# Performance work log

Hardware: AMD Instinct MI355X
Metric: run time of the kernel (lower is better)

The kernel has to match this reference:

```python
import jax, jax.numpy as jnp
import numpy as np

DT = 0.001
TAU_SYN = 0.01
TAU_MEM = 0.005
THRESHOLD = 1.0
ALPHA = float(np.exp(-DT / TAU_SYN))  # syn decay
BETA = float(np.exp(-DT / TAU_MEM))   # mem decay

BATCH, IN_SIZE, OUT_SIZE = 4096, 2048, 2048


@jax.custom_vjp
def spike(x):
    # Heaviside forward with sigmoid-derivative surrogate gradient
    return (x > 0).astype(x.dtype)

def _spike_fwd(x):
    return spike(x), x

def _spike_bwd(x, g):
    s = jax.nn.sigmoid(x)
    return (g * s * (1.0 - s),)

spike.defvjp(_spike_fwd, _spike_bwd)


def setup_inputs() -> dict:
    key = jax.random.key(0)
    k1, k2, k3, k4, k5 = jax.random.split(key, 5)
    inputs = jax.random.normal(k1, (BATCH, IN_SIZE), dtype=jnp.float32)
    I = jax.random.normal(k2, (BATCH, OUT_SIZE), dtype=jnp.float32)
    V = jax.random.normal(k3, (BATCH, OUT_SIZE), dtype=jnp.float32)
    Z = jnp.zeros((BATCH, OUT_SIZE), dtype=jnp.float32)
    # initialize_weights_: ndim<=2 -> normal init
    fwd_w = jax.random.normal(k4, (IN_SIZE, OUT_SIZE), dtype=jnp.float32)
    rec_w = jax.random.normal(k5, (OUT_SIZE, OUT_SIZE), dtype=jnp.float32)
    return {"inputs": inputs, "I": I, "V": V, "Z": Z,
            "fwd_w": fwd_w, "rec_w": rec_w}


def reference(inputs, I, V, Z, fwd_w, rec_w):
    # LIFLayer.forward_Erme, single timestep
    input_current = jnp.matmul(inputs, fwd_w)          # [B, O]
    rec_current = jnp.matmul(Z, rec_w)                 # [B, O]
    is_active = 1.0 - jax.lax.stop_gradient(Z)
    next_I = ALPHA * I + input_current + rec_current
    next_V = (BETA * V + next_I) * is_active
    next_Z = spike(next_V - THRESHOLD)
    return next_Z, next_I, next_V
```

## Files before the change

kernel.cpp:

```cpp
#include <hip/hip_runtime.h>
#include <cstdint>
#include <cstddef>

typedef __bf16 bf16_t;
typedef __bf16 bf16x4 __attribute__((ext_vector_type(4)));
typedef __bf16 bf16x8 __attribute__((ext_vector_type(8)));
typedef float f32x4 __attribute__((ext_vector_type(4)));

#define M_DIM 4096
#define K_DIM 2048
#define N_DIM 2048

#define BM 128
#define BN 128
#define BK 64
#define KT (K_DIM / BK)
#define A_EL (BM * BK)
#define B_EL (BN * BK)
#define PER_BUF (A_EL + B_EL)
#define B_OFF A_EL

#define ZCAP 64

#define MFMA16(a, b, c) \
  __builtin_amdgcn_mfma_f32_16x16x32_bf16((a), (b), (c), 0, 0, 0)

__device__ __forceinline__ void gload_lds16(const bf16_t* g, bf16_t* l) {
  __builtin_amdgcn_global_load_lds(
      (const __attribute__((address_space(1))) void*)g,
      (__attribute__((address_space(3))) void*)l, 16, 0, 0);
}

__global__ __launch_bounds__(256) void prepass_all(
    const float* __restrict__ inputs, const float* __restrict__ fwd_w,
    const float* __restrict__ Z, bf16_t* __restrict__ abf,
    bf16_t* __restrict__ wT, int* __restrict__ zcnt, int* __restrict__ zidx,
    float* __restrict__ zval) {
  __shared__ float tile[64][65];
  const int b = blockIdx.x;
  const int t = threadIdx.x;

  if (b < 4096) {
    const size_t base = ((size_t)b * 256 + t) * 8;
    const float4 v0 = *reinterpret_cast<const float4*>(inputs + base);
    const float4 v1 = *reinterpret_cast<const float4*>(inputs + base + 4);
    bf16x8 o;
    o[0] = (bf16_t)v0.x; o[1] = (bf16_t)v0.y;
    o[2] = (bf16_t)v0.z; o[3] = (bf16_t)v0.w;
    o[4] = (bf16_t)v1.x; o[5] = (bf16_t)v1.y;
    o[6] = (bf16_t)v1.z; o[7] = (bf16_t)v1.w;
    *reinterpret_cast<bf16x8*>(abf + base) = o;
  } else if (b < 5120) {
    const int bb = b - 4096;
    const int n0 = (bb & 31) * 64;
    const int k0 = (bb >> 5) * 64;
#pragma unroll
    for (int p = 0; p < 4; ++p) {
      const int r = p * 16 + (t >> 4);
      const int c = (t & 15) * 4;
      const float4 v = *reinterpret_cast<const float4*>(
          &fwd_w[(size_t)(k0 + r) * N_DIM + n0 + c]);
      tile[r][c + 0] = v.x;
      tile[r][c + 1] = v.y;
      tile[r][c + 2] = v.z;
      tile[r][c + 3] = v.w;
    }
    __syncthreads();
#pragma unroll
    for (int p = 0; p < 4; ++p) {
      const int n = p * 16 + (t >> 4);
      const int c = (t & 15) * 4;
      bf16x4 o;
      o[0] = (bf16_t)tile[c + 0][n];
      o[1] = (bf16_t)tile[c + 1][n];
      o[2] = (bf16_t)tile[c + 2][n];
      o[3] = (bf16_t)tile[c + 3][n];
      *reinterpret_cast<bf16x4*>(&wT[(size_t)(n0 + n) * K_DIM + k0 + c]) = o;
    }
  } else {
    const int row = (b - 5120) * 4 + (t >> 6);
    const int lane = t & 63;
    const float* zr = Z + (size_t)row * N_DIM;
    int local = 0;
#pragma unroll
    for (int c = 0; c < 32; c += 4) {
      const f32x4 v = *reinterpret_cast<const f32x4*>(zr + lane * 32 + c);
#pragma unroll
      for (int e = 0; e < 4; ++e) local += (v[e] != 0.0f) ? 1 : 0;
    }
    int pre = local;
#pragma unroll
    for (int d = 1; d < 64; d <<= 1) {
      const int up = __shfl_up(pre, d, 64);
      if (lane >= d) pre += up;
    }
    const int total = __shfl(pre, 63, 64);
    if (lane == 0) zcnt[row] = total;
    if (total > 0 && total <= ZCAP) {
      int wpos = pre - local;
      int* zi = zidx + (size_t)row * ZCAP;
      float* zv = zval + (size_t)row * ZCAP;
      for (int c = lane * 32; c < lane * 32 + 32; ++c) {
        const float v = zr[c];
        if (v != 0.0f) {
          zi[wpos] = c;
          zv[wpos] = v;
          ++wpos;
        }
      }
    }
  }
}

__global__ __launch_bounds__(256, 2) void lif_gemm_db(
    const bf16_t* __restrict__ A, const bf16_t* __restrict__ W,
    const float* __restrict__ recw,
    const int* __restrict__ zcnt, const int* __restrict__ zidx,
    const float* __restrict__ zval,
    const float* __restrict__ Iin, const float* __restrict__ Vin,
    const float* __restrict__ Zin,
    float* __restrict__ outZ, float* __restrict__ outI,
    float* __restrict__ outV) {
  __shared__ __align__(16) bf16_t lds[2 * PER_BUF];

  const int tid = threadIdx.x;
  const int lane = tid & 63;
  const int wave = tid >> 6;
  const int wm = wave >> 1;
  const int wn = wave & 1;
  const int l15 = lane & 15;
  const int l4 = lane >> 4;

  const int bid = blockIdx.x;
  const int swz = (bid & 7) * 64 + (bid >> 3);
  const int m0 = (swz >> 4) * BM;
  const int n0 = (swz & 15) * BN;

  const int lr = lane >> 3;
  const int sg = (lane & 7) ^ lr;
  const bf16_t* aSrc[4];
  const bf16_t* bSrc[4];
  int aDst[4], bDst[4];
#pragma unroll
  for (int i = 0; i < 4; ++i) {
    const int r = wave * 32 + i * 8 + lr;
    aSrc[i] = A + (size_t)(m0 + r) * K_DIM + sg * 8;
    aDst[i] = r * BK + (lane & 7) * 8;
    bSrc[i] = W + (size_t)(n0 + r) * K_DIM + sg * 8;
    bDst[i] = B_OFF + r * BK + (lane & 7) * 8;
  }

  int aBase[2], bBase[2];
#pragma unroll
  for (int ks = 0; ks < 2; ++ks) {
    const int phys = (l4 + ks * 4) ^ (l15 & 7);
    aBase[ks] = (wm * 64 + l15) * BK + phys * 8;
    bBase[ks] = B_OFF + (wn * 64 + l15) * BK + phys * 8;
  }

  f32x4 acc[4][4];
#pragma unroll
  for (int i = 0; i < 4; ++i)
#pragma unroll
    for (int j = 0; j < 4; ++j)
#pragma unroll
      for (int e = 0; e < 4; ++e) acc[i][j][e] = 0.0f;

#pragma unroll
  for (int i = 0; i < 4; ++i) {
    gload_lds16(aSrc[i], lds + aDst[i]);
    gload_lds16(bSrc[i], lds + bDst[i]);
  }
#pragma unroll
  for (int i = 0; i < 4; ++i) {
    gload_lds16(aSrc[i] + BK, lds + PER_BUF + aDst[i]);
    gload_lds16(bSrc[i] + BK, lds + PER_BUF + bDst[i]);
  }
  asm volatile("s_waitcnt vmcnt(8)" ::: "memory");
  __builtin_amdgcn_sched_barrier(0);
  __builtin_amdgcn_s_barrier();
  __builtin_amdgcn_sched_barrier(0);

  for (int t = 0; t < KT; ++t) {
    const bf16_t* bufC = lds + (t & 1) * PER_BUF;
    bf16_t* bufS = lds + (t & 1) * PER_BUF;

    bf16x8 af[4][2], bfr[4][2];
#pragma unroll
    for (int mi = 0; mi < 4; ++mi)
#pragma unroll
      for (int ks = 0; ks < 2; ++ks)
        af[mi][ks] =
            *reinterpret_cast<const bf16x8*>(bufC + aBase[ks] + mi * 1024);
#pragma unroll
    for (int ni = 0; ni < 4; ++ni)
#pragma unroll
      for (int ks = 0; ks < 2; ++ks)
        bfr[ni][ks] =
            *reinterpret_cast<const bf16x8*>(bufC + bBase[ks] + ni * 1024);
    asm volatile("s_waitcnt lgkmcnt(0)" ::: "memory");
    __builtin_amdgcn_sched_barrier(0);
    __builtin_amdgcn_s_barrier();
    __builtin_amdgcn_sched_barrier(0);

    if (t + 2 < KT) {
      const int kt = (t + 2) * BK;
#pragma unroll
      for (int i = 0; i < 4; ++i) {
        gload_lds16(aSrc[i] + kt, bufS + aDst[i]);
        gload_lds16(bSrc[i] + kt, bufS + bDst[i]);
      }
    }

    __builtin_amdgcn_s_setprio(1);
#pragma unroll
    for (int mi = 0; mi < 4; ++mi)
#pragma unroll
      for (int ni = 0; ni < 4; ++ni) {
        acc[mi][ni] = MFMA16(af[mi][0], bfr[ni][0], acc[mi][ni]);
        acc[mi][ni] = MFMA16(af[mi][1], bfr[ni][1], acc[mi][ni]);
      }
    __builtin_amdgcn_s_setprio(0);
    __builtin_amdgcn_sched_barrier(0);

    if (t + 2 < KT) {
      asm volatile("s_waitcnt vmcnt(8)" ::: "memory");
    } else if (t + 1 < KT) {
      asm volatile("s_waitcnt vmcnt(0)" ::: "memory");
    }
    __builtin_amdgcn_sched_barrier(0);
    __builtin_amdgcn_s_barrier();
    __builtin_amdgcn_sched_barrier(0);
  }

  const float alpha = 0.90483741803595957f;
  const float beta = 0.81873075307798182f;
  float* swp = reinterpret_cast<float*>(lds) + wave * (16 * 66);
  const int er = lane >> 2;
  const int ec = (lane & 3) * 4;

#pragma unroll
  for (int mi = 0; mi < 4; ++mi) {
#pragma unroll
    for (int ni = 0; ni < 4; ++ni)
#pragma unroll
      for (int j = 0; j < 4; ++j)
        swp[(l4 * 4 + j) * 66 + ni * 16 + l15] = acc[mi][ni][j];

    const int row = m0 + wm * 64 + mi * 16 + er;
    const int colb = n0 + wn * 64 + ec;
    const int cnt = zcnt[row];

    f32x4 rec4[4], gate4[4];
#pragma unroll
    for (int cc = 0; cc < 4; ++cc)
#pragma unroll
      for (int e = 0; e < 4; ++e) {
        rec4[cc][e] = 0.0f;
        gate4[cc][e] = 1.0f;
      }
    if (cnt > 0) {
      if (cnt <= ZCAP) {
        const int* zi = zidx + (size_t)row * ZCAP;
        const float* zv = zval + (size_t)row * ZCAP;
        for (int s = 0; s < cnt; ++s) {
          const int o = zi[s];
          const float v = zv[s];
          const float* wr = recw + (size_t)o * N_DIM + colb;
#pragma unroll
          for (int cc = 0; cc < 4; ++cc) {
            const f32x4 wv = *reinterpret_cast<const f32x4*>(wr + cc * 16);
#pragma unroll
            for (int e = 0; e < 4; ++e) {
              rec4[cc][e] += v * wv[e];
              gate4[cc][e] = (o == colb + cc * 16 + e) ? (1.0f - v)
                                                       : gate4[cc][e];
            }
          }
        }
      } else {
        const float* zr = Zin + (size_t)row * N_DIM;
        for (int o = 0; o < N_DIM; ++o) {
          const float v = zr[o];
          if (v != 0.0f) {
            const float* wr = recw + (size_t)o * N_DIM + colb;
#pragma unroll
            for (int cc = 0; cc < 4; ++cc) {
              const f32x4 wv = *reinterpret_cast<const f32x4*>(wr + cc * 16);
#pragma unroll
              for (int e = 0; e < 4; ++e) {
                rec4[cc][e] += v * wv[e];
                gate4[cc][e] = (o == colb + cc * 16 + e) ? (1.0f - v)
                                                         : gate4[cc][e];
              }
            }
          }
        }
      }
    }

    const size_t gb = (size_t)row * N_DIM + colb;
#pragma unroll
    for (int cc = 0; cc < 4; ++cc) {
      const f32x4 av =
          *reinterpret_cast<const f32x4*>(swp + er * 66 + ec + cc * 16);
      const f32x4 iv = *reinterpret_cast<const f32x4*>(Iin + gb + cc * 16);
      const f32x4 vv = *reinterpret_cast<const f32x4*>(Vin + gb + cc * 16);
      f32x4 nI, nV, nZ;
#pragma unroll
      for (int e = 0; e < 4; ++e) {
        nI[e] = alpha * iv[e] + av[e] + rec4[cc][e];
        nV[e] = (beta * vv[e] + nI[e]) * gate4[cc][e];
        nZ[e] = (nV[e] > 1.0f) ? 1.0f : 0.0f;
      }
      *reinterpret_cast<f32x4*>(outI + gb + cc * 16) = nI;
      *reinterpret_cast<f32x4*>(outV + gb + cc * 16) = nV;
      *reinterpret_cast<f32x4*>(outZ + gb + cc * 16) = nZ;
    }
  }
}

extern "C" void kernel_launch(void* const* d_in, const int* in_sizes, int n_in,
                              void* d_out, int out_size, void* d_ws,
                              size_t ws_size, hipStream_t stream) {
  const float* inputs = (const float*)d_in[0];
  const float* I = (const float*)d_in[1];
  const float* V = (const float*)d_in[2];
  const float* Z = (const float*)d_in[3];
  const float* fwd_w = (const float*)d_in[4];
  const float* rec_w = (const float*)d_in[5];

  float* outZ = (float*)d_out;
  float* outI = outZ + (size_t)M_DIM * N_DIM;
  float* outV = outI + (size_t)M_DIM * N_DIM;

  bf16_t* abf = (bf16_t*)d_ws;
  bf16_t* wT = (bf16_t*)((char*)d_ws + (size_t)M_DIM * K_DIM * 2);
  char* p = (char*)d_ws + (size_t)M_DIM * K_DIM * 2 + (size_t)N_DIM * K_DIM * 2;
  int* zcnt = (int*)p;
  int* zidx = (int*)(p + M_DIM * 4);
  float* zval = (float*)(p + M_DIM * 4 + (size_t)M_DIM * ZCAP * 4);

  hipLaunchKernelGGL(prepass_all, dim3(6144), dim3(256), 0, stream, inputs,
                     fwd_w, Z, abf, wT, zcnt, zidx, zval);
  hipLaunchKernelGGL(lif_gemm_db, dim3((M_DIM / BM) * (N_DIM / BN)),
                     dim3(256), 0, stream, abf, wT, rec_w, zcnt, zidx, zval, I,
                     V, Z, outZ, outI, outV);
}
```

Measured before the change: 85.87 us.

## Replace 4-wave 128x128 GEMM tiles with single-wave 64x64 tiles

```diff
diff --git a/kernel.cpp b/kernel.cpp
--- a/kernel.cpp
+++ b/kernel.cpp
@@ -11,13 +11,12 @@
 #define K_DIM 2048
 #define N_DIM 2048
 
-#define BM 128
-#define BN 128
+#define BM 64
+#define BN 64
 #define BK 64
 #define KT (K_DIM / BK)
 #define A_EL (BM * BK)
 #define B_EL (BN * BK)
-#define PER_BUF (A_EL + B_EL)
 #define B_OFF A_EL
 
 #define ZCAP 64
@@ -112,7 +111,7 @@
   }
 }
 
-__global__ __launch_bounds__(256, 2) void lif_gemm_db(
+__global__ __launch_bounds__(64, 2) void lif_gemm_1w(
     const bf16_t* __restrict__ A, const bf16_t* __restrict__ W,
     const float* __restrict__ recw,
     const int* __restrict__ zcnt, const int* __restrict__ zidx,
@@ -121,41 +120,30 @@
     const float* __restrict__ Zin,
     float* __restrict__ outZ, float* __restrict__ outI,
     float* __restrict__ outV) {
-  __shared__ __align__(16) bf16_t lds[2 * PER_BUF];
-
-  const int tid = threadIdx.x;
-  const int lane = tid & 63;
-  const int wave = tid >> 6;
-  const int wm = wave >> 1;
-  const int wn = wave & 1;
+  __shared__ __align__(16) bf16_t lds[A_EL + B_EL];
+
+  const int lane = threadIdx.x;
   const int l15 = lane & 15;
   const int l4 = lane >> 4;
 
   const int bid = blockIdx.x;
-  const int swz = (bid & 7) * 64 + (bid >> 3);
-  const int m0 = (swz >> 4) * BM;
-  const int n0 = (swz & 15) * BN;
+  const int swz = (bid & 7) * 256 + (bid >> 3);
+  const int m0 = (swz >> 5) * BM;
+  const int n0 = (swz & 31) * BN;
 
   const int lr = lane >> 3;
-  const int sg = (lane & 7) ^ lr;
-  const bf16_t* aSrc[4];
-  const bf16_t* bSrc[4];
-  int aDst[4], bDst[4];
-#pragma unroll
-  for (int i = 0; i < 4; ++i) {
-    const int r = wave * 32 + i * 8 + lr;
-    aSrc[i] = A + (size_t)(m0 + r) * K_DIM + sg * 8;
-    aDst[i] = r * BK + (lane & 7) * 8;
-    bSrc[i] = W + (size_t)(n0 + r) * K_DIM + sg * 8;
-    bDst[i] = B_OFF + r * BK + (lane & 7) * 8;
-  }
+  const int sl = lane & 7;
+  const int sg = sl ^ lr;
+  const bf16_t* aS = A + (size_t)(m0 + lr) * K_DIM + sg * 8;
+  const bf16_t* bS = W + (size_t)(n0 + lr) * K_DIM + sg * 8;
+  const int dst = lr * BK + sl * 8;
 
   int aBase[2], bBase[2];
 #pragma unroll
   for (int ks = 0; ks < 2; ++ks) {
     const int phys = (l4 + ks * 4) ^ (l15 & 7);
-    aBase[ks] = (wm * 64 + l15) * BK + phys * 8;
-    bBase[ks] = B_OFF + (wn * 64 + l15) * BK + phys * 8;
+    aBase[ks] = l15 * BK + phys * 8;
+    bBase[ks] = B_OFF + l15 * BK + phys * 8;
   }
 
   f32x4 acc[4][4];
@@ -167,50 +155,40 @@
       for (int e = 0; e < 4; ++e) acc[i][j][e] = 0.0f;
 
 #pragma unroll
-  for (int i = 0; i < 4; ++i) {
-    gload_lds16(aSrc[i], lds + aDst[i]);
-    gload_lds16(bSrc[i], lds + bDst[i]);
-  }
-#pragma unroll
-  for (int i = 0; i < 4; ++i) {
-    gload_lds16(aSrc[i] + BK, lds + PER_BUF + aDst[i]);
-    gload_lds16(bSrc[i] + BK, lds + PER_BUF + bDst[i]);
-  }
-  asm volatile("s_waitcnt vmcnt(8)" ::: "memory");
+  for (int i = 0; i < 8; ++i) {
+    gload_lds16(aS + (size_t)i * 8 * K_DIM, lds + dst + i * 512);
+    gload_lds16(bS + (size_t)i * 8 * K_DIM, lds + B_OFF + dst + i * 512);
+  }
+  asm volatile("s_waitcnt vmcnt(0)" ::: "memory");
   __builtin_amdgcn_sched_barrier(0);
-  __builtin_amdgcn_s_barrier();
-  __builtin_amdgcn_sched_barrier(0);
 
   for (int t = 0; t < KT; ++t) {
-    const bf16_t* bufC = lds + (t & 1) * PER_BUF;
-    bf16_t* bufS = lds + (t & 1) * PER_BUF;
-
     bf16x8 af[4][2], bfr[4][2];
 #pragma unroll
     for (int mi = 0; mi < 4; ++mi)
 #pragma unroll
       for (int ks = 0; ks < 2; ++ks)
         af[mi][ks] =
-            *reinterpret_cast<const bf16x8*>(bufC + aBase[ks] + mi * 1024);
+            *reinterpret_cast<const bf16x8*>(lds + aBase[ks] + mi * 1024);
 #pragma unroll
     for (int ni = 0; ni < 4; ++ni)
 #pragma unroll
       for (int ks = 0; ks < 2; ++ks)
         bfr[ni][ks] =
-            *reinterpret_cast<const bf16x8*>(bufC + bBase[ks] + ni * 1024);
+            *reinterpret_cast<const bf16x8*>(lds + bBase[ks] + ni * 1024);
     asm volatile("s_waitcnt lgkmcnt(0)" ::: "memory");
     __builtin_amdgcn_sched_barrier(0);
-    __builtin_amdgcn_s_barrier();
+
+    if (t + 1 < KT) {
+      const int kt = (t + 1) * BK;
+#pragma unroll
+      for (int i = 0; i < 8; ++i) {
+        gload_lds16(aS + kt + (size_t)i * 8 * K_DIM, lds + dst + i * 512);
+        gload_lds16(bS + kt + (size_t)i * 8 * K_DIM,
+                    lds + B_OFF + dst + i * 512);
+      }
+    }
     __builtin_amdgcn_sched_barrier(0);
-
-    if (t + 2 < KT) {
-      const int kt = (t + 2) * BK;
-#pragma unroll
-      for (int i = 0; i < 4; ++i) {
-        gload_lds16(aSrc[i] + kt, bufS + aDst[i]);
-        gload_lds16(bSrc[i] + kt, bufS + bDst[i]);
-      }
-    }
 
     __builtin_amdgcn_s_setprio(1);
 #pragma unroll
@@ -223,19 +201,15 @@
     __builtin_amdgcn_s_setprio(0);
     __builtin_amdgcn_sched_barrier(0);
 
-    if (t + 2 < KT) {
-      asm volatile("s_waitcnt vmcnt(8)" ::: "memory");
-    } else if (t + 1 < KT) {
+    if (t + 1 < KT) {
       asm volatile("s_waitcnt vmcnt(0)" ::: "memory");
-    }
-    __builtin_amdgcn_sched_barrier(0);
-    __builtin_amdgcn_s_barrier();
-    __builtin_amdgcn_sched_barrier(0);
+      __builtin_amdgcn_sched_barrier(0);
+    }
   }
 
   const float alpha = 0.90483741803595957f;
   const float beta = 0.81873075307798182f;
-  float* swp = reinterpret_cast<float*>(lds) + wave * (16 * 66);
+  float* swp = reinterpret_cast<float*>(lds);
   const int er = lane >> 2;
   const int ec = (lane & 3) * 4;
 
@@ -247,8 +221,8 @@
       for (int j = 0; j < 4; ++j)
         swp[(l4 * 4 + j) * 66 + ni * 16 + l15] = acc[mi][ni][j];
 
-    const int row = m0 + wm * 64 + mi * 16 + er;
-    const int colb = n0 + wn * 64 + ec;
+    const int row = m0 + mi * 16 + er;
+    const int colb = n0 + ec;
     const int cnt = zcnt[row];
 
     f32x4 rec4[4], gate4[4];
@@ -343,7 +317,7 @@
 
   hipLaunchKernelGGL(prepass_all, dim3(6144), dim3(256), 0, stream, inputs,
                      fwd_w, Z, abf, wT, zcnt, zidx, zval);
-  hipLaunchKernelGGL(lif_gemm_db, dim3((M_DIM / BM) * (N_DIM / BN)),
-                     dim3(256), 0, stream, abf, wT, rec_w, zcnt, zidx, zval, I,
-                     V, Z, outZ, outI, outV);
+  hipLaunchKernelGGL(lif_gemm_1w, dim3((M_DIM / BM) * (N_DIM / BN)), dim3(64),
+                     0, stream, abf, wT, rec_w, zcnt, zidx, zval, I, V, Z,
+                     outZ, outI, outV);
 }
```

Result: slower. 102.4 us (+19.3%).

## Replace double-buffered LDS pipeline with single-buffer load-sync-compute loop

Applied to the files above, without the earlier changes.

```diff
diff --git a/kernel.cpp b/kernel.cpp
--- a/kernel.cpp
+++ b/kernel.cpp
@@ -17,7 +17,6 @@
 #define KT (K_DIM / BK)
 #define A_EL (BM * BK)
 #define B_EL (BN * BK)
-#define PER_BUF (A_EL + B_EL)
 #define B_OFF A_EL
 
 #define ZCAP 64
@@ -112,7 +111,7 @@
   }
 }
 
-__global__ __launch_bounds__(256, 2) void lif_gemm_db(
+__global__ __launch_bounds__(256, 2) void lif_gemm_m97(
     const bf16_t* __restrict__ A, const bf16_t* __restrict__ W,
     const float* __restrict__ recw,
     const int* __restrict__ zcnt, const int* __restrict__ zidx,
@@ -121,7 +120,7 @@
     const float* __restrict__ Zin,
     float* __restrict__ outZ, float* __restrict__ outI,
     float* __restrict__ outV) {
-  __shared__ __align__(16) bf16_t lds[2 * PER_BUF];
+  __shared__ __align__(16) bf16_t lds[A_EL + B_EL];
 
   const int tid = threadIdx.x;
   const int lane = tid & 63;
@@ -166,24 +165,14 @@
 #pragma unroll
       for (int e = 0; e < 4; ++e) acc[i][j][e] = 0.0f;
 
-#pragma unroll
-  for (int i = 0; i < 4; ++i) {
-    gload_lds16(aSrc[i], lds + aDst[i]);
-    gload_lds16(bSrc[i], lds + bDst[i]);
-  }
-#pragma unroll
-  for (int i = 0; i < 4; ++i) {
-    gload_lds16(aSrc[i] + BK, lds + PER_BUF + aDst[i]);
-    gload_lds16(bSrc[i] + BK, lds + PER_BUF + bDst[i]);
-  }
-  asm volatile("s_waitcnt vmcnt(8)" ::: "memory");
-  __builtin_amdgcn_sched_barrier(0);
-  __builtin_amdgcn_s_barrier();
-  __builtin_amdgcn_sched_barrier(0);
-
   for (int t = 0; t < KT; ++t) {
-    const bf16_t* bufC = lds + (t & 1) * PER_BUF;
-    bf16_t* bufS = lds + (t & 1) * PER_BUF;
+    const int kt = t * BK;
+#pragma unroll
+    for (int i = 0; i < 4; ++i) {
+      gload_lds16(aSrc[i] + kt, lds + aDst[i]);
+      gload_lds16(bSrc[i] + kt, lds + bDst[i]);
+    }
+    __syncthreads();
 
     bf16x8 af[4][2], bfr[4][2];
 #pragma unroll
@@ -191,28 +180,13 @@
 #pragma unroll
       for (int ks = 0; ks < 2; ++ks)
         af[mi][ks] =
-            *reinterpret_cast<const bf16x8*>(bufC + aBase[ks] + mi * 1024);
+            *reinterpret_cast<const bf16x8*>(lds + aBase[ks] + mi * 1024);
 #pragma unroll
     for (int ni = 0; ni < 4; ++ni)
 #pragma unroll
       for (int ks = 0; ks < 2; ++ks)
         bfr[ni][ks] =
-            *reinterpret_cast<const bf16x8*>(bufC + bBase[ks] + ni * 1024);
-    asm volatile("s_waitcnt lgkmcnt(0)" ::: "memory");
-    __builtin_amdgcn_sched_barrier(0);
-    __builtin_amdgcn_s_barrier();
-    __builtin_amdgcn_sched_barrier(0);
-
-    if (t + 2 < KT) {
-      const int kt = (t + 2) * BK;
-#pragma unroll
-      for (int i = 0; i < 4; ++i) {
-        gload_lds16(aSrc[i] + kt, bufS + aDst[i]);
-        gload_lds16(bSrc[i] + kt, bufS + bDst[i]);
-      }
-    }
-
-    __builtin_amdgcn_s_setprio(1);
+            *reinterpret_cast<const bf16x8*>(lds + bBase[ks] + ni * 1024);
 #pragma unroll
     for (int mi = 0; mi < 4; ++mi)
 #pragma unroll
@@ -220,17 +194,7 @@
         acc[mi][ni] = MFMA16(af[mi][0], bfr[ni][0], acc[mi][ni]);
         acc[mi][ni] = MFMA16(af[mi][1], bfr[ni][1], acc[mi][ni]);
       }
-    __builtin_amdgcn_s_setprio(0);
-    __builtin_amdgcn_sched_barrier(0);
-
-    if (t + 2 < KT) {
-      asm volatile("s_waitcnt vmcnt(8)" ::: "memory");
-    } else if (t + 1 < KT) {
-      asm volatile("s_waitcnt vmcnt(0)" ::: "memory");
-    }
-    __builtin_amdgcn_sched_barrier(0);
-    __builtin_amdgcn_s_barrier();
-    __builtin_amdgcn_sched_barrier(0);
+    __syncthreads();
   }
 
   const float alpha = 0.90483741803595957f;
@@ -343,7 +307,7 @@
 
   hipLaunchKernelGGL(prepass_all, dim3(6144), dim3(256), 0, stream, inputs,
                      fwd_w, Z, abf, wT, zcnt, zidx, zval);
-  hipLaunchKernelGGL(lif_gemm_db, dim3((M_DIM / BM) * (N_DIM / BN)),
+  hipLaunchKernelGGL(lif_gemm_m97, dim3((M_DIM / BM) * (N_DIM / BN)),
                      dim3(256), 0, stream, abf, wT, rec_w, zcnt, zidx, zval, I,
                      V, Z, outZ, outI, outV);
 }
```

Result: slower. 92.44 us (+7.6%).
